# Kernel optimization log

Measured on AMD Instinct MI355X. Metric: run time of the kernel, lower is better.

## Reference

```python
import jax, jax.numpy as jnp
import numpy as np

N = 100000      # num mesh nodes
E = 600000      # num directed edges (avg degree ~6)
IN = 6          # input features
HID = 128       # hidden channels
HEADS = 8
CH = HID // HEADS  # 16 per-head channels
L = 4           # num GNN layers
OUT = 4


def layer_norm(x, w, b, eps=1e-5):
    m = x.mean(-1, keepdims=True)
    v = ((x - m) ** 2).mean(-1, keepdims=True)
    return (x - m) / jnp.sqrt(v + eps) * w + b


def setup_inputs() -> dict:
    key = jax.random.key(0)
    ks = jax.random.split(key, 24)
    s = 0.05
    inp = {
        "x": jax.random.normal(ks[0], (N, IN), jnp.float32),
        "edge_index": jax.random.randint(ks[1], (2, E), 0, N, jnp.int64),
        # input MLP: Linear(IN,HID) + LayerNorm
        "w_in": jax.random.normal(ks[2], (IN, HID), jnp.float32) * s,
        "b_in": jnp.zeros((HID,), jnp.float32),
        "ln_in_w": jnp.ones((HID,), jnp.float32),
        "ln_in_b": jnp.zeros((HID,), jnp.float32),
        # 4 GAT layers (stacked): W, att_src, att_dst, bias + per-layer LayerNorm
        "Wg": jax.random.normal(ks[3], (L, HID, HID), jnp.float32) * s,
        "a_src": jax.random.normal(ks[4], (L, HEADS, CH), jnp.float32) * s,
        "a_dst": jax.random.normal(ks[5], (L, HEADS, CH), jnp.float32) * s,
        "bg": jnp.zeros((L, HID), jnp.float32),
        "lnw": jnp.ones((L, HID), jnp.float32),
        "lnb": jnp.zeros((L, HID), jnp.float32),
        # output MLP: Linear(HID,HID)+LN+ReLU -> Linear(HID,HID//2)+ReLU -> Linear(HID//2,OUT)
        "w1": jax.random.normal(ks[6], (HID, HID), jnp.float32) * s,
        "b1": jnp.zeros((HID,), jnp.float32),
        "lnow": jnp.ones((HID,), jnp.float32),
        "lnob": jnp.zeros((HID,), jnp.float32),
        "w2": jax.random.normal(ks[7], (HID, HID // 2), jnp.float32) * s,
        "b2": jnp.zeros((HID // 2,), jnp.float32),
        "w3": jax.random.normal(ks[8], (HID // 2, OUT), jnp.float32) * s,
        "b3": jnp.zeros((OUT,), jnp.float32),
    }
    return inp


def reference(x, edge_index, w_in, b_in, ln_in_w, ln_in_b,
              Wg, a_src, a_dst, bg, lnw, lnb,
              w1, b1, lnow, lnob, w2, b2, w3, b3):
    # PyG GATConv adds self-loops by default
    loop = jnp.arange(N, dtype=edge_index.dtype)
    src = jnp.concatenate([edge_index[0], loop])  # message source
    dst = jnp.concatenate([edge_index[1], loop])  # message destination (softmax groups)

    h = jax.nn.relu(layer_norm(x @ w_in + b_in, ln_in_w, ln_in_b))  # (N, HID); dropout off (eval)

    for i in range(L):
        xw = (h @ Wg[i]).reshape(N, HEADS, CH)            # per-head transform
        al_s = (xw * a_src[i]).sum(-1)                    # (N, HEADS)
        al_d = (xw * a_dst[i]).sum(-1)                    # (N, HEADS)
        e = jax.nn.leaky_relu(al_s[src] + al_d[dst], 0.2) # (E+N, HEADS)
        # numerically stable segment softmax over incoming edges of each dst
        mx = jax.ops.segment_max(e, dst, num_segments=N)
        p = jnp.exp(e - mx[dst])
        denom = jax.ops.segment_sum(p, dst, num_segments=N)
        alpha = p / denom[dst]                            # attention dropout off (eval)
        msg = xw[src] * alpha[:, :, None]                 # (E+N, HEADS, CH)
        agg = jax.ops.segment_sum(msg, dst, num_segments=N).reshape(N, HID) + bg[i]
        h = h + jax.nn.relu(layer_norm(agg, lnw[i], lnb[i]))

    o = jax.nn.relu(layer_norm(h @ w1 + b1, lnow, lnob))
    o = jax.nn.relu(o @ w2 + b2)
    return o @ w3 + b3
```

## Files before the change

### kernel.cpp

```cpp
#include <hip/hip_runtime.h>
#include <hip/hip_bf16.h>

#define NN 100000
#define NE 600000

typedef __bf16 bf16x8 __attribute__((ext_vector_type(8)));
typedef __bf16 bf16x4 __attribute__((ext_vector_type(4)));
typedef float  f32x4  __attribute__((ext_vector_type(4)));

__device__ __forceinline__ float dot4(float4 a, float4 b){
  return a.x*b.x + a.y*b.y + a.z*b.z + a.w*b.w;
}
__device__ __forceinline__ void bf2f(unsigned v, float& a, float& b){
  union { unsigned u; float f; } ua, ub;
  ua.u = v << 16;
  ub.u = v & 0xFFFF0000u;
  a = ua.f; b = ub.f;
}
__device__ __forceinline__ void bf8f(uint4 v, float* r){
  bf2f(v.x, r[0], r[1]);
  bf2f(v.y, r[2], r[3]);
  bf2f(v.z, r[4], r[5]);
  bf2f(v.w, r[6], r[7]);
}

__global__ void count_edges(const int* __restrict__ dst, int* __restrict__ cnt){
  int e = blockIdx.x*256 + threadIdx.x;
  if (e < NE){
    unsigned d = (unsigned)dst[e];
    if (d < NN) atomicAdd(&cnt[d], 1);
  }
}

__global__ void scan1(const int* __restrict__ cnt, int* __restrict__ offs, int* __restrict__ bsum){
  __shared__ int sh[256];
  const int tid = threadIdx.x;
  const int base = blockIdx.x*2048 + tid*8;
  int pre[8]; int s = 0;
  #pragma unroll
  for (int j=0;j<8;j++){
    int idx = base + j;
    int v = (idx < NN) ? cnt[idx] : 0;
    pre[j] = s; s += v;
  }
  sh[tid] = s;
  __syncthreads();
  for (int d=1; d<256; d<<=1){
    int t = (tid >= d) ? sh[tid-d] : 0;
    __syncthreads();
    sh[tid] += t;
    __syncthreads();
  }
  int off = (tid > 0) ? sh[tid-1] : 0;
  #pragma unroll
  for (int j=0;j<8;j++){
    int idx = base + j;
    if (idx < NN) offs[idx] = off + pre[j];
  }
  if (tid == 255) bsum[blockIdx.x] = sh[255];
}

__global__ void scan2(int* __restrict__ bsum){
  if (threadIdx.x == 0){
    int s = 0;
    for (int i=0;i<49;i++){ int t = bsum[i]; bsum[i] = s; s += t; }
  }
}

__global__ void scan3(int* __restrict__ offs, const int* __restrict__ bsum, int* __restrict__ cursor){
  int i = blockIdx.x*256 + threadIdx.x;
  if (i < NN){
    int v = offs[i] + bsum[i>>11];
    offs[i] = v; cursor[i] = v;
  }
  if (i == 0) offs[NN] = NE;
}

__global__ void fill_csr(const int* __restrict__ src, const int* __restrict__ dst,
                         int* __restrict__ cursor, int* __restrict__ csrsrc){
  int e = blockIdx.x*256 + threadIdx.x;
  if (e < NE){
    unsigned d = (unsigned)dst[e];
    unsigned s = (unsigned)src[e];
    if (d < NN && s < NN){
      int p = atomicAdd(&cursor[d], 1);
      csrsrc[p] = (int)s;
    }
  }
}

__global__ void repack_w(const float* __restrict__ Wg, const float* __restrict__ w1,
                         const float* __restrict__ w2,
                         __bf16* __restrict__ phi, __bf16* __restrict__ plo)
{
  int gid = blockIdx.x*256 + threadIdx.x;
  const float* W; int C; size_t obase; int rem;
  if (gid < 8192)      { W = Wg + (size_t)(gid/2048)*16384; C = 128; obase = (size_t)(gid/2048)*16384; rem = gid % 2048; }
  else if (gid < 10240){ W = w1; C = 128; obase = 65536; rem = gid - 8192; }
  else if (gid < 11264){ W = w2; C = 64;  obase = 81920; rem = gid - 10240; }
  else return;
  const int lane = rem & 63;
  const int tks  = rem >> 6;
  const int ks = tks & 3, t = tks >> 2;
  const int col = t*16 + (lane & 15);
  const int kb  = ks*32 + (lane >> 4)*8;
  const size_t o = obase + (size_t)rem*8;
  #pragma unroll
  for (int j=0;j<8;j++){
    float v = W[(size_t)(kb+j)*C + col];
    __bf16 hb = (__bf16)v;
    phi[o+j] = hb;
    plo[o+j] = (__bf16)(v - (float)hb);
  }
}

__global__ __launch_bounds__(256) void input_mlp(const float* __restrict__ x,
    const float* __restrict__ win, const float* __restrict__ b,
    const float* __restrict__ lnw, const float* __restrict__ lnb,
    __bf16* __restrict__ h)
{
  const int tid = threadIdx.x;
  const int g = tid >> 5, l = tid & 31;
  const int n = blockIdx.x*8 + g;
  const float4* W4 = (const float4*)win;
  float xr[6];
  #pragma unroll
  for (int k=0;k<6;k++) xr[k] = x[n*6+k];
  float4 s = ((const float4*)b)[l];
  #pragma unroll
  for (int k=0;k<6;k++){
    float4 w = W4[k*32 + l];
    s.x = fmaf(xr[k], w.x, s.x);
    s.y = fmaf(xr[k], w.y, s.y);
    s.z = fmaf(xr[k], w.z, s.z);
    s.w = fmaf(xr[k], w.w, s.w);
  }
  float sum = s.x+s.y+s.z+s.w;
  float sq  = dot4(s,s);
  #pragma unroll
  for (int o=16;o>=1;o>>=1){ sum += __shfl_xor(sum,o); sq += __shfl_xor(sq,o); }
  float mean = sum*(1.f/128.f);
  float var  = sq*(1.f/128.f) - mean*mean;
  float rr = rsqrtf(var + 1e-5f);
  float4 lw = ((const float4*)lnw)[l];
  float4 lb = ((const float4*)lnb)[l];
  bf16x4 y;
  y[0] = (__bf16)fmaxf((s.x-mean)*rr*lw.x + lb.x, 0.f);
  y[1] = (__bf16)fmaxf((s.y-mean)*rr*lw.y + lb.y, 0.f);
  y[2] = (__bf16)fmaxf((s.z-mean)*rr*lw.z + lb.z, 0.f);
  y[3] = (__bf16)fmaxf((s.w-mean)*rr*lw.w + lb.w, 0.f);
  *(bf16x4*)(h + (size_t)n*128 + 4*l) = y;
}

template<int C, bool HAS_BIAS, bool DO_LN, bool DO_RELU, bool GAT, bool OUTP, bool SPLIT, bool SKIPLO, bool ABF16>
__global__ __launch_bounds__(256) void gemm_mfma(
    const float* __restrict__ Xf, const __bf16* __restrict__ Xb,
    const __bf16* __restrict__ Bhi, const __bf16* __restrict__ Blo,
    const float* __restrict__ bias,
    const float* __restrict__ lnw, const float* __restrict__ lnb,
    const float* __restrict__ asrc, const float* __restrict__ adst,
    float* __restrict__ Y, __bf16* __restrict__ Yb,
    float* __restrict__ als, float* __restrict__ ald,
    const float* __restrict__ w3, const float* __restrict__ b3,
    float* __restrict__ outp)
{
  constexpr int NT = SPLIT ? C/32 : C/16;
  const int tid = threadIdx.x;
  const int wid = tid >> 6, lane = tid & 63;
  const int lrow = lane & 15, lgrp = lane >> 4;
  const int m0    = SPLIT ? (blockIdx.x*32 + (wid>>1)*16) : ((blockIdx.x*4 + wid)*16);
  const int colt0 = SPLIT ? (wid & 1)*NT : 0;

  bf16x8 Ahi[4], Alo[4];
  {
    int row = m0 + lrow; if (row >= NN) row = NN-1;
    if constexpr (ABF16){
      const __bf16* Xr = Xb + (size_t)row*128 + lgrp*8;
      #pragma unroll
      for (int ks=0; ks<4; ks++) Ahi[ks] = *(const bf16x8*)(Xr + ks*32);
    } else {
      const float* Xr = Xf + (size_t)row*128 + lgrp*8;
      #pragma unroll
      for (int ks=0; ks<4; ks++){
        float4 u0 = *(const float4*)(Xr + ks*32);
        float4 u1 = *(const float4*)(Xr + ks*32 + 4);
        float v[8] = {u0.x,u0.y,u0.z,u0.w,u1.x,u1.y,u1.z,u1.w};
        bf16x8 h8, l8;
        #pragma unroll
        for (int j=0;j<8;j++){
          __bf16 hb = (__bf16)v[j];
          h8[j] = hb;
          l8[j] = (__bf16)(v[j] - (float)hb);
        }
        Ahi[ks] = h8; Alo[ks] = l8;
      }
    }
  }

  f32x4 acc[NT];
  #pragma unroll
  for (int t=0;t<NT;t++){ acc[t] = (f32x4){0.f,0.f,0.f,0.f}; }

  const bf16x8* B8h = (const bf16x8*)Bhi;
  const bf16x8* B8l = (const bf16x8*)Blo;
  #pragma unroll
  for (int ks=0;ks<4;ks++){
    bf16x8 bh[NT];
    #pragma unroll
    for (int t=0;t<NT;t++) bh[t] = B8h[((colt0+t)*4+ks)*64 + lane];
    #pragma unroll
    for (int t=0;t<NT;t++)
      acc[t] = __builtin_amdgcn_mfma_f32_16x16x32_bf16(Ahi[ks], bh[t], acc[t], 0,0,0);
    if constexpr (!ABF16){
      #pragma unroll
      for (int t=0;t<NT;t++)
        acc[t] = __builtin_amdgcn_mfma_f32_16x16x32_bf16(Alo[ks], bh[t], acc[t], 0,0,0);
    }
    if constexpr (!SKIPLO){
      #pragma unroll
      for (int t=0;t<NT;t++){
        bf16x8 bl = B8l[((colt0+t)*4+ks)*64 + lane];
        acc[t] = __builtin_amdgcn_mfma_f32_16x16x32_bf16(Ahi[ks], bl, acc[t], 0,0,0);
      }
    }
  }

  if constexpr (HAS_BIAS){
    #pragma unroll
    for (int t=0;t<NT;t++){
      float bv = bias[(colt0+t)*16 + lrow];
      #pragma unroll
      for (int i=0;i<4;i++) acc[t][i] += bv;
    }
  }

  if constexpr (GAT){
    #pragma unroll
    for (int t=0;t<NT;t++){
      float av = asrc[(colt0+t)*16 + lrow];
      float dv2 = adst[(colt0+t)*16 + lrow];
      float ps[4], pd[4];
      #pragma unroll
      for (int i=0;i<4;i++){
        int n = m0 + lgrp*4 + i;
        if (n < NN) Yb[(size_t)n*C + (colt0+t)*16 + lrow] = (__bf16)acc[t][i];
        ps[i] = acc[t][i]*av; pd[i] = acc[t][i]*dv2;
      }
      #pragma unroll
      for (int off=1; off<16; off<<=1){
        #pragma unroll
        for (int i=0;i<4;i++){
          ps[i] += __shfl_xor(ps[i], off);
          pd[i] += __shfl_xor(pd[i], off);
        }
      }
      if (lrow == 0){
        #pragma unroll
        for (int i=0;i<4;i++){
          int n = m0 + lgrp*4 + i;
          if (n < NN){ als[n*8 + colt0 + t] = ps[i]; ald[n*8 + colt0 + t] = pd[i]; }
        }
      }
    }
  } else {
    if constexpr (DO_LN){
      float s[4] = {0,0,0,0}, q[4] = {0,0,0,0};
      #pragma unroll
      for (int t=0;t<NT;t++){
        #pragma unroll
        for (int i=0;i<4;i++){ s[i] += acc[t][i]; q[i] += acc[t][i]*acc[t][i]; }
      }
      #pragma unroll
      for (int off=1; off<16; off<<=1){
        #pragma unroll
        for (int i=0;i<4;i++){ s[i] += __shfl_xor(s[i], off); q[i] += __shfl_xor(q[i], off); }
      }
      float mean[4], rr[4];
      #pragma unroll
      for (int i=0;i<4;i++){
        mean[i] = s[i]*(1.0f/C);
        float var = q[i]*(1.0f/C) - mean[i]*mean[i];
        rr[i] = rsqrtf(var + 1e-5f);
      }
      #pragma unroll
      for (int t=0;t<NT;t++){
        float lw = lnw[t*16 + lrow], lb = lnb[t*16 + lrow];
        #pragma unroll
        for (int i=0;i<4;i++){
          float v = (acc[t][i]-mean[i])*rr[i]*lw + lb;
          if constexpr (DO_RELU) v = fmaxf(v, 0.f);
          acc[t][i] = v;
        }
      }
    } else if constexpr (DO_RELU){
      #pragma unroll
      for (int t=0;t<NT;t++){
        #pragma unroll
        for (int i=0;i<4;i++) acc[t][i] = fmaxf(acc[t][i], 0.f);
      }
    }
    if constexpr (OUTP){
      float4 w3r[NT];
      #pragma unroll
      for (int t=0;t<NT;t++) w3r[t] = ((const float4*)w3)[t*16 + lrow];
      float4 b3v = *(const float4*)b3;
      #pragma unroll
      for (int i=0;i<4;i++){
        float4 po = make_float4(0.f,0.f,0.f,0.f);
        #pragma unroll
        for (int t=0;t<NT;t++){
          po.x = fmaf(acc[t][i], w3r[t].x, po.x);
          po.y = fmaf(acc[t][i], w3r[t].y, po.y);
          po.z = fmaf(acc[t][i], w3r[t].z, po.z);
          po.w = fmaf(acc[t][i], w3r[t].w, po.w);
        }
        #pragma unroll
        for (int off=1; off<16; off<<=1){
          po.x += __shfl_xor(po.x, off);
          po.y += __shfl_xor(po.y, off);
          po.z += __shfl_xor(po.z, off);
          po.w += __shfl_xor(po.w, off);
        }
        if (lrow == 0){
          int n = m0 + lgrp*4 + i;
          if (n < NN){
            float4 o;
            o.x = po.x + b3v.x; o.y = po.y + b3v.y;
            o.z = po.z + b3v.z; o.w = po.w + b3v.w;
            ((float4*)outp)[n] = o;
          }
        }
      }
    } else {
      #pragma unroll
      for (int t=0;t<NT;t++){
        #pragma unroll
        for (int i=0;i<4;i++){
          int n = m0 + lgrp*4 + i;
          if (n < NN) Y[(size_t)n*C + t*16 + lrow] = acc[t][i];
        }
      }
    }
  }
}

__global__ __launch_bounds__(256) void gat_aggregate(
    const __bf16* __restrict__ xw, const float* __restrict__ als, const float* __restrict__ ald,
    const int* __restrict__ offs, const int* __restrict__ csrsrc,
    const float* __restrict__ bg, const float* __restrict__ lnw, const float* __restrict__ lnb,
    __bf16* __restrict__ h)
{
  const int tid = threadIdx.x;
  const int grp = tid >> 4, sl = tid & 15;
  const int n = blockIdx.x*16 + grp;
  const int hh = sl >> 1;
  const float ad = ald[n*8 + hh];
  const uint4* xw128 = (const uint4*)xw;

  float t = als[n*8 + hh] + ad; t = t > 0.f ? t : 0.2f*t;
  float pp = __expf(t);
  float s = pp;
  float m[8];
  bf8f(xw128[(unsigned)n*16u + sl], m);
  float acc[8];
  #pragma unroll
  for (int c=0;c<8;c++) acc[c] = pp*m[c];

  const int start = offs[n], end = offs[n+1];
  int e = start;
  for (; e+4 <= end; e += 4){
    int s4[4]; float a[4]; uint4 x4[4];
    #pragma unroll
    for (int j=0;j<4;j++) s4[j] = csrsrc[e+j];
    #pragma unroll
    for (int j=0;j<4;j++){
      a[j]  = als[s4[j]*8 + hh];
      x4[j] = xw128[(unsigned)s4[j]*16u + sl];
    }
    #pragma unroll
    for (int j=0;j<4;j++){
      float u = a[j] + ad; u = u > 0.f ? u : 0.2f*u;
      float q = __expf(u);
      s += q;
      float mm[8];
      bf8f(x4[j], mm);
      #pragma unroll
      for (int c=0;c<8;c++) acc[c] = fmaf(q, mm[c], acc[c]);
    }
  }
  if (e+2 <= end){
    int sA = csrsrc[e], sB = csrsrc[e+1];
    float aA = als[sA*8+hh], aB = als[sB*8+hh];
    uint4 xA = xw128[(unsigned)sA*16u + sl];
    uint4 xB = xw128[(unsigned)sB*16u + sl];
    float u;
    u = aA+ad; u = u>0.f?u:0.2f*u; float qA = __expf(u);
    u = aB+ad; u = u>0.f?u:0.2f*u; float qB = __expf(u);
    s += qA+qB;
    float mA[8], mB[8];
    bf8f(xA, mA); bf8f(xB, mB);
    #pragma unroll
    for (int c=0;c<8;c++) acc[c] = fmaf(qA, mA[c], fmaf(qB, mB[c], acc[c]));
    e += 2;
  }
  if (e < end){
    int sA = csrsrc[e];
    float aA = als[sA*8+hh];
    uint4 xA = xw128[(unsigned)sA*16u + sl];
    float u = aA+ad; u = u>0.f?u:0.2f*u; float qA = __expf(u);
    s += qA;
    float mA[8];
    bf8f(xA, mA);
    #pragma unroll
    for (int c=0;c<8;c++) acc[c] = fmaf(qA, mA[c], acc[c]);
  }

  float4 bg0 = ((const float4*)bg)[2*sl];
  float4 bg1 = ((const float4*)bg)[2*sl+1];
  float bgv[8] = {bg0.x,bg0.y,bg0.z,bg0.w,bg1.x,bg1.y,bg1.z,bg1.w};
  float inv = 1.0f/s;
  float val[8];
  #pragma unroll
  for (int c=0;c<8;c++) val[c] = acc[c]*inv + bgv[c];
  float sum = 0.f, sq = 0.f;
  #pragma unroll
  for (int c=0;c<8;c++){ sum += val[c]; sq += val[c]*val[c]; }
  #pragma unroll
  for (int off=8; off>=1; off>>=1){ sum += __shfl_xor(sum,off); sq += __shfl_xor(sq,off); }
  float mean = sum*(1.f/128.f);
  float var  = sq*(1.f/128.f) - mean*mean;
  float rr = rsqrtf(var + 1e-5f);
  float4 lw0 = ((const float4*)lnw)[2*sl];
  float4 lw1 = ((const float4*)lnw)[2*sl+1];
  float4 lb0 = ((const float4*)lnb)[2*sl];
  float4 lb1 = ((const float4*)lnb)[2*sl+1];
  float lwv[8] = {lw0.x,lw0.y,lw0.z,lw0.w,lw1.x,lw1.y,lw1.z,lw1.w};
  float lbv[8] = {lb0.x,lb0.y,lb0.z,lb0.w,lb1.x,lb1.y,lb1.z,lb1.w};
  bf16x8* hp = (bf16x8*)(h + (size_t)n*128 + 8*sl);
  bf16x8 hv8 = *hp;
  bf16x8 ho;
  #pragma unroll
  for (int c=0;c<8;c++){
    float hv = (float)hv8[c] + fmaxf((val[c]-mean)*rr*lwv[c] + lbv[c], 0.f);
    ho[c] = (__bf16)hv;
  }
  *hp = ho;
}

extern "C" void kernel_launch(void* const* d_in, const int* in_sizes, int n_in,
                              void* d_out, int out_size, void* d_ws, size_t ws_size,
                              hipStream_t stream)
{
  const float* x       = (const float*)d_in[0];
  const int*   ei      = (const int*)d_in[1];
  const float* w_in    = (const float*)d_in[2];
  const float* b_in    = (const float*)d_in[3];
  const float* ln_in_w = (const float*)d_in[4];
  const float* ln_in_b = (const float*)d_in[5];
  const float* Wg      = (const float*)d_in[6];
  const float* a_src   = (const float*)d_in[7];
  const float* a_dst   = (const float*)d_in[8];
  const float* bg      = (const float*)d_in[9];
  const float* lnw     = (const float*)d_in[10];
  const float* lnb     = (const float*)d_in[11];
  const float* w1      = (const float*)d_in[12];
  const float* b1      = (const float*)d_in[13];
  const float* lnow    = (const float*)d_in[14];
  const float* lnob    = (const float*)d_in[15];
  const float* w2      = (const float*)d_in[16];
  const float* b2      = (const float*)d_in[17];
  const float* w3      = (const float*)d_in[18];
  const float* b3      = (const float*)d_in[19];
  float* out = (float*)d_out;

  char* p = (char*)d_ws;
  auto carve = [&](size_t bytes)->void*{
    void* r = (void*)p; p += (bytes + 255) & ~(size_t)255; return r;
  };
  __bf16* h   = (__bf16*)carve((size_t)NN*128*2);
  float* xw   = (float*)carve((size_t)NN*128*4);
  __bf16* xwb = (__bf16*)carve((size_t)NN*128*2);
  float* als  = (float*)carve((size_t)NN*8*4);
  float* ald  = (float*)carve((size_t)NN*8*4);
  int* offs   = (int*)carve((size_t)(NN+1)*4);
  int* cursor = (int*)carve((size_t)NN*4);
  int* cnt    = (int*)carve((size_t)NN*4);
  int* csrsrc = (int*)carve((size_t)NE*4);
  int* bsum   = (int*)carve(64*4);
  __bf16* pWhi = (__bf16*)carve((size_t)90112*2);
  __bf16* pWlo = (__bf16*)carve((size_t)90112*2);

  const int* esrc = ei;
  const int* edst = ei + NE;

  repack_w<<<44, 256, 0, stream>>>(Wg, w1, w2, pWhi, pWlo);

  hipMemsetAsync(cnt, 0, (size_t)NN*4, stream);
  count_edges<<<(NE+255)/256, 256, 0, stream>>>(edst, cnt);
  scan1<<<49, 256, 0, stream>>>(cnt, offs, bsum);
  scan2<<<1, 64, 0, stream>>>(bsum);
  scan3<<<(NN+255)/256, 256, 0, stream>>>(offs, bsum, cursor);
  fill_csr<<<(NE+255)/256, 256, 0, stream>>>(esrc, edst, cursor, csrsrc);

  input_mlp<<<NN/8, 256, 0, stream>>>(x, w_in, b_in, ln_in_w, ln_in_b, h);

  const int GRID  = (NN + 63) / 64;
  const int GRIDS = (NN + 31) / 32;
  for (int i=0;i<4;i++){
    gemm_mfma<128,false,false,false,true,false,true,true,true><<<GRIDS, 256, 0, stream>>>(
        nullptr, h, pWhi + (size_t)i*16384, pWlo + (size_t)i*16384, nullptr, nullptr, nullptr,
        a_src + i*128, a_dst + i*128, nullptr, xwb, als, ald, nullptr, nullptr, nullptr);
    gat_aggregate<<<NN/16, 256, 0, stream>>>(xwb, als, ald, offs, csrsrc,
        bg + i*128, lnw + i*128, lnb + i*128, h);
  }

  gemm_mfma<128,true,true,true,false,false,false,false,true><<<GRID, 256, 0, stream>>>(
      nullptr, h, pWhi + 65536, pWlo + 65536, b1, lnow, lnob, nullptr, nullptr, xw, nullptr,
      nullptr, nullptr, nullptr, nullptr, nullptr);
  gemm_mfma<64,true,false,true,false,true,false,false,false><<<GRID, 256, 0, stream>>>(
      xw, nullptr, pWhi + 81920, pWlo + 81920, b2, nullptr, nullptr, nullptr, nullptr, nullptr, nullptr,
      nullptr, nullptr, w3, b3, out);
}
```

Baseline: 411.4 us.

## Fold attention vectors into GAT weight and use 32x32 MFMA GEMM

Precomputes W·a_src and W·a_dst as 16 extra output columns of the per-layer weight, so the attention logits come straight out of the GEMM instead of being reduced with shuffles. The GAT projection moves to a new kernel built on 32x32x16 bf16 MFMA, with 128 rows per block and a fifth column tile holding the logits. The goal is to cut the epilogue shuffle work and raise MFMA efficiency. In exchange it does extra padded MFMA work on the logit tile, and the folded attention weights are rounded to bf16, which changes precision.

```diff
diff --git a/kernel.cpp b/kernel.cpp
--- a/kernel.cpp
+++ b/kernel.cpp
@@ -7,6 +7,7 @@
 typedef __bf16 bf16x8 __attribute__((ext_vector_type(8)));
 typedef __bf16 bf16x4 __attribute__((ext_vector_type(4)));
 typedef float  f32x4  __attribute__((ext_vector_type(4)));
+typedef float  f32x16 __attribute__((ext_vector_type(16)));
 
 __device__ __forceinline__ float dot4(float4 a, float4 b){
   return a.x*b.x + a.y*b.y + a.z*b.z + a.w*b.w;
@@ -114,6 +115,40 @@
   }
 }
 
+__global__ void repack_w32(const float* __restrict__ Wg,
+                           const float* __restrict__ a_src, const float* __restrict__ a_dst,
+                           __bf16* __restrict__ pb)
+{
+  int gid = blockIdx.x*256 + threadIdx.x;
+  if (gid >= 10240) return;
+  const int layer = gid / 2560, rem = gid % 2560;
+  const float* W = Wg + (size_t)layer*16384;
+  const int lane = rem & 63;
+  const int tks  = rem >> 6;
+  const int ks = tks & 7, t = tks >> 3;
+  const int kb  = ks*16 + (lane >> 5)*8;
+  const size_t o = (size_t)layer*20480 + (size_t)rem*8;
+  if (t < 4){
+    const int col = t*32 + (lane & 31);
+    #pragma unroll
+    for (int j=0;j<8;j++) pb[o+j] = (__bf16)W[(size_t)(kb+j)*128 + col];
+  } else {
+    const int cc = lane & 31;
+    #pragma unroll
+    for (int j=0;j<8;j++){
+      float v = 0.f;
+      if (cc < 16){
+        const int hd = cc & 7;
+        const float* av = (cc < 8 ? a_src : a_dst) + layer*128 + hd*16;
+        const int k = kb + j;
+        #pragma unroll
+        for (int c=0;c<16;c++) v += W[(size_t)k*128 + hd*16 + c] * av[c];
+      }
+      pb[o+j] = (__bf16)v;
+    }
+  }
+}
+
 __global__ __launch_bounds__(256) void input_mlp(const float* __restrict__ x,
     const float* __restrict__ win, const float* __restrict__ b,
     const float* __restrict__ lnw, const float* __restrict__ lnb,
@@ -152,24 +187,72 @@
   *(bf16x4*)(h + (size_t)n*128 + 4*l) = y;
 }
 
-template<int C, bool HAS_BIAS, bool DO_LN, bool DO_RELU, bool GAT, bool OUTP, bool SPLIT, bool SKIPLO, bool ABF16>
+__global__ __launch_bounds__(256) void gemm32_gat(const __bf16* __restrict__ X,
+    const __bf16* __restrict__ B32,
+    __bf16* __restrict__ Yb, float* __restrict__ als, float* __restrict__ ald)
+{
+  const int tid = threadIdx.x;
+  const int wid = tid >> 6, lane = tid & 63;
+  const int lm = lane & 31, lh = lane >> 5;
+  const int m0 = blockIdx.x*128 + wid*32;
+
+  f32x16 acc[5];
+  #pragma unroll
+  for (int t=0;t<5;t++){
+    #pragma unroll
+    for (int i=0;i<16;i++) acc[t][i] = 0.f;
+  }
+
+  int row = m0 + lm; if (row >= NN) row = NN-1;
+  const __bf16* Xr = X + (size_t)row*128 + lh*8;
+  const bf16x8* B8 = (const bf16x8*)B32;
+
+  #pragma unroll
+  for (int ks=0; ks<8; ks++){
+    bf16x8 a = *(const bf16x8*)(Xr + ks*16);
+    bf16x8 bh[5];
+    #pragma unroll
+    for (int t=0;t<5;t++) bh[t] = B8[(t*8+ks)*64 + lane];
+    #pragma unroll
+    for (int t=0;t<5;t++)
+      acc[t] = __builtin_amdgcn_mfma_f32_32x32x16_bf16(a, bh[t], acc[t], 0,0,0);
+  }
+
+  #pragma unroll
+  for (int t=0;t<4;t++){
+    #pragma unroll
+    for (int i=0;i<16;i++){
+      int r = (i&3) + 8*(i>>2) + 4*lh;
+      int n = m0 + r;
+      if (n < NN) Yb[(size_t)n*128 + t*32 + lm] = (__bf16)acc[t][i];
+    }
+  }
+  #pragma unroll
+  for (int i=0;i<16;i++){
+    int r = (i&3) + 8*(i>>2) + 4*lh;
+    int n = m0 + r;
+    if (n < NN){
+      if (lm < 8)       als[n*8 + lm]     = acc[4][i];
+      else if (lm < 16) ald[n*8 + lm - 8] = acc[4][i];
+    }
+  }
+}
+
+template<int C, bool DO_LN, bool DO_RELU, bool OUTP, bool ABF16>
 __global__ __launch_bounds__(256) void gemm_mfma(
     const float* __restrict__ Xf, const __bf16* __restrict__ Xb,
     const __bf16* __restrict__ Bhi, const __bf16* __restrict__ Blo,
     const float* __restrict__ bias,
     const float* __restrict__ lnw, const float* __restrict__ lnb,
-    const float* __restrict__ asrc, const float* __restrict__ adst,
-    float* __restrict__ Y, __bf16* __restrict__ Yb,
-    float* __restrict__ als, float* __restrict__ ald,
+    float* __restrict__ Y,
     const float* __restrict__ w3, const float* __restrict__ b3,
     float* __restrict__ outp)
 {
-  constexpr int NT = SPLIT ? C/32 : C/16;
+  constexpr int NT = C/16;
   const int tid = threadIdx.x;
   const int wid = tid >> 6, lane = tid & 63;
   const int lrow = lane & 15, lgrp = lane >> 4;
-  const int m0    = SPLIT ? (blockIdx.x*32 + (wid>>1)*16) : ((blockIdx.x*4 + wid)*16);
-  const int colt0 = SPLIT ? (wid & 1)*NT : 0;
+  const int m0 = (blockIdx.x*4 + wid)*16;
 
   bf16x8 Ahi[4], Alo[4];
   {
@@ -207,7 +290,7 @@
   for (int ks=0;ks<4;ks++){
     bf16x8 bh[NT];
     #pragma unroll
-    for (int t=0;t<NT;t++) bh[t] = B8h[((colt0+t)*4+ks)*64 + lane];
+    for (int t=0;t<NT;t++) bh[t] = B8h[(t*4+ks)*64 + lane];
     #pragma unroll
     for (int t=0;t<NT;t++)
       acc[t] = __builtin_amdgcn_mfma_f32_16x16x32_bf16(Ahi[ks], bh[t], acc[t], 0,0,0);
@@ -216,129 +299,97 @@
       for (int t=0;t<NT;t++)
         acc[t] = __builtin_amdgcn_mfma_f32_16x16x32_bf16(Alo[ks], bh[t], acc[t], 0,0,0);
     }
-    if constexpr (!SKIPLO){
+    {
       #pragma unroll
       for (int t=0;t<NT;t++){
-        bf16x8 bl = B8l[((colt0+t)*4+ks)*64 + lane];
+        bf16x8 bl = B8l[(t*4+ks)*64 + lane];
         acc[t] = __builtin_amdgcn_mfma_f32_16x16x32_bf16(Ahi[ks], bl, acc[t], 0,0,0);
       }
     }
   }
 
-  if constexpr (HAS_BIAS){
+  #pragma unroll
+  for (int t=0;t<NT;t++){
+    float bv = bias[t*16 + lrow];
+    #pragma unroll
+    for (int i=0;i<4;i++) acc[t][i] += bv;
+  }
+
+  if constexpr (DO_LN){
+    float s[4] = {0,0,0,0}, q[4] = {0,0,0,0};
     #pragma unroll
     for (int t=0;t<NT;t++){
-      float bv = bias[(colt0+t)*16 + lrow];
-      #pragma unroll
-      for (int i=0;i<4;i++) acc[t][i] += bv;
-    }
-  }
-
-  if constexpr (GAT){
+      #pragma unroll
+      for (int i=0;i<4;i++){ s[i] += acc[t][i]; q[i] += acc[t][i]*acc[t][i]; }
+    }
+    #pragma unroll
+    for (int off=1; off<16; off<<=1){
+      #pragma unroll
+      for (int i=0;i<4;i++){ s[i] += __shfl_xor(s[i], off); q[i] += __shfl_xor(q[i], off); }
+    }
+    float mean[4], rr[4];
+    #pragma unroll
+    for (int i=0;i<4;i++){
+      mean[i] = s[i]*(1.0f/C);
+      float var = q[i]*(1.0f/C) - mean[i]*mean[i];
+      rr[i] = rsqrtf(var + 1e-5f);
+    }
     #pragma unroll
     for (int t=0;t<NT;t++){
-      float av = asrc[(colt0+t)*16 + lrow];
-      float dv2 = adst[(colt0+t)*16 + lrow];
-      float ps[4], pd[4];
+      float lw = lnw[t*16 + lrow], lb = lnb[t*16 + lrow];
+      #pragma unroll
+      for (int i=0;i<4;i++){
+        float v = (acc[t][i]-mean[i])*rr[i]*lw + lb;
+        if constexpr (DO_RELU) v = fmaxf(v, 0.f);
+        acc[t][i] = v;
+      }
+    }
+  } else if constexpr (DO_RELU){
+    #pragma unroll
+    for (int t=0;t<NT;t++){
+      #pragma unroll
+      for (int i=0;i<4;i++) acc[t][i] = fmaxf(acc[t][i], 0.f);
+    }
+  }
+  if constexpr (OUTP){
+    float4 w3r[NT];
+    #pragma unroll
+    for (int t=0;t<NT;t++) w3r[t] = ((const float4*)w3)[t*16 + lrow];
+    float4 b3v = *(const float4*)b3;
+    #pragma unroll
+    for (int i=0;i<4;i++){
+      float4 po = make_float4(0.f,0.f,0.f,0.f);
+      #pragma unroll
+      for (int t=0;t<NT;t++){
+        po.x = fmaf(acc[t][i], w3r[t].x, po.x);
+        po.y = fmaf(acc[t][i], w3r[t].y, po.y);
+        po.z = fmaf(acc[t][i], w3r[t].z, po.z);
+        po.w = fmaf(acc[t][i], w3r[t].w, po.w);
+      }
+      #pragma unroll
+      for (int off=1; off<16; off<<=1){
+        po.x += __shfl_xor(po.x, off);
+        po.y += __shfl_xor(po.y, off);
+        po.z += __shfl_xor(po.z, off);
+        po.w += __shfl_xor(po.w, off);
+      }
+      if (lrow == 0){
+        int n = m0 + lgrp*4 + i;
+        if (n < NN){
+          float4 o;
+          o.x = po.x + b3v.x; o.y = po.y + b3v.y;
+          o.z = po.z + b3v.z; o.w = po.w + b3v.w;
+          ((float4*)outp)[n] = o;
+        }
+      }
+    }
+  } else {
+    #pragma unroll
+    for (int t=0;t<NT;t++){
       #pragma unroll
       for (int i=0;i<4;i++){
         int n = m0 + lgrp*4 + i;
-        if (n < NN) Yb[(size_t)n*C + (colt0+t)*16 + lrow] = (__bf16)acc[t][i];
-        ps[i] = acc[t][i]*av; pd[i] = acc[t][i]*dv2;
-      }
-      #pragma unroll
-      for (int off=1; off<16; off<<=1){
-        #pragma unroll
-        for (int i=0;i<4;i++){
-          ps[i] += __shfl_xor(ps[i], off);
-          pd[i] += __shfl_xor(pd[i], off);
-        }
-      }
-      if (lrow == 0){
-        #pragma unroll
-        for (int i=0;i<4;i++){
-          int n = m0 + lgrp*4 + i;
-          if (n < NN){ als[n*8 + colt0 + t] = ps[i]; ald[n*8 + colt0 + t] = pd[i]; }
-        }
-      }
-    }
-  } else {
-    if constexpr (DO_LN){
-      float s[4] = {0,0,0,0}, q[4] = {0,0,0,0};
-      #pragma unroll
-      for (int t=0;t<NT;t++){
-        #pragma unroll
-        for (int i=0;i<4;i++){ s[i] += acc[t][i]; q[i] += acc[t][i]*acc[t][i]; }
-      }
-      #pragma unroll
-      for (int off=1; off<16; off<<=1){
-        #pragma unroll
-        for (int i=0;i<4;i++){ s[i] += __shfl_xor(s[i], off); q[i] += __shfl_xor(q[i], off); }
-      }
-      float mean[4], rr[4];
-      #pragma unroll
-      for (int i=0;i<4;i++){
-        mean[i] = s[i]*(1.0f/C);
-        float var = q[i]*(1.0f/C) - mean[i]*mean[i];
-        rr[i] = rsqrtf(var + 1e-5f);
-      }
-      #pragma unroll
-      for (int t=0;t<NT;t++){
-        float lw = lnw[t*16 + lrow], lb = lnb[t*16 + lrow];
-        #pragma unroll
-        for (int i=0;i<4;i++){
-          float v = (acc[t][i]-mean[i])*rr[i]*lw + lb;
-          if constexpr (DO_RELU) v = fmaxf(v, 0.f);
-          acc[t][i] = v;
-        }
-      }
-    } else if constexpr (DO_RELU){
-      #pragma unroll
-      for (int t=0;t<NT;t++){
-        #pragma unroll
-        for (int i=0;i<4;i++) acc[t][i] = fmaxf(acc[t][i], 0.f);
-      }
-    }
-    if constexpr (OUTP){
-      float4 w3r[NT];
-      #pragma unroll
-      for (int t=0;t<NT;t++) w3r[t] = ((const float4*)w3)[t*16 + lrow];
-      float4 b3v = *(const float4*)b3;
-      #pragma unroll
-      for (int i=0;i<4;i++){
-        float4 po = make_float4(0.f,0.f,0.f,0.f);
-        #pragma unroll
-        for (int t=0;t<NT;t++){
-          po.x = fmaf(acc[t][i], w3r[t].x, po.x);
-          po.y = fmaf(acc[t][i], w3r[t].y, po.y);
-          po.z = fmaf(acc[t][i], w3r[t].z, po.z);
-          po.w = fmaf(acc[t][i], w3r[t].w, po.w);
-        }
-        #pragma unroll
-        for (int off=1; off<16; off<<=1){
-          po.x += __shfl_xor(po.x, off);
-          po.y += __shfl_xor(po.y, off);
-          po.z += __shfl_xor(po.z, off);
-          po.w += __shfl_xor(po.w, off);
-        }
-        if (lrow == 0){
-          int n = m0 + lgrp*4 + i;
-          if (n < NN){
-            float4 o;
-            o.x = po.x + b3v.x; o.y = po.y + b3v.y;
-            o.z = po.z + b3v.z; o.w = po.w + b3v.w;
-            ((float4*)outp)[n] = o;
-          }
-        }
-      }
-    } else {
-      #pragma unroll
-      for (int t=0;t<NT;t++){
-        #pragma unroll
-        for (int i=0;i<4;i++){
-          int n = m0 + lgrp*4 + i;
-          if (n < NN) Y[(size_t)n*C + t*16 + lrow] = acc[t][i];
-        }
+        if (n < NN) Y[(size_t)n*C + t*16 + lrow] = acc[t][i];
       }
     }
   }
@@ -489,11 +540,13 @@
   int* bsum   = (int*)carve(64*4);
   __bf16* pWhi = (__bf16*)carve((size_t)90112*2);
   __bf16* pWlo = (__bf16*)carve((size_t)90112*2);
+  __bf16* pW32 = (__bf16*)carve((size_t)4*20480*2);
 
   const int* esrc = ei;
   const int* edst = ei + NE;
 
   repack_w<<<44, 256, 0, stream>>>(Wg, w1, w2, pWhi, pWlo);
+  repack_w32<<<40, 256, 0, stream>>>(Wg, a_src, a_dst, pW32);
 
   hipMemsetAsync(cnt, 0, (size_t)NN*4, stream);
   count_edges<<<(NE+255)/256, 256, 0, stream>>>(edst, cnt);
@@ -504,20 +557,17 @@
 
   input_mlp<<<NN/8, 256, 0, stream>>>(x, w_in, b_in, ln_in_w, ln_in_b, h);
 
-  const int GRID  = (NN + 63) / 64;
-  const int GRIDS = (NN + 31) / 32;
+  const int GRID   = (NN + 63) / 64;
+  const int GRID32 = (NN + 127) / 128;
   for (int i=0;i<4;i++){
-    gemm_mfma<128,false,false,false,true,false,true,true,true><<<GRIDS, 256, 0, stream>>>(
-        nullptr, h, pWhi + (size_t)i*16384, pWlo + (size_t)i*16384, nullptr, nullptr, nullptr,
-        a_src + i*128, a_dst + i*128, nullptr, xwb, als, ald, nullptr, nullptr, nullptr);
+    gemm32_gat<<<GRID32, 256, 0, stream>>>(
+        h, pW32 + (size_t)i*20480, xwb, als, ald);
     gat_aggregate<<<NN/16, 256, 0, stream>>>(xwb, als, ald, offs, csrsrc,
         bg + i*128, lnw + i*128, lnb + i*128, h);
   }
 
-  gemm_mfma<128,true,true,true,false,false,false,false,true><<<GRID, 256, 0, stream>>>(
-      nullptr, h, pWhi + 65536, pWlo + 65536, b1, lnow, lnob, nullptr, nullptr, xw, nullptr,
-      nullptr, nullptr, nullptr, nullptr, nullptr);
-  gemm_mfma<64,true,false,true,false,true,false,false,false><<<GRID, 256, 0, stream>>>(
-      xw, nullptr, pWhi + 81920, pWlo + 81920, b2, nullptr, nullptr, nullptr, nullptr, nullptr, nullptr,
-      nullptr, nullptr, w3, b3, out);
-}
+  gemm_mfma<128,true,true,false,true><<<GRID, 256, 0, stream>>>(
+      nullptr, h, pWhi + 65536, pWlo + 65536, b1, lnow, lnob, xw, nullptr, nullptr, nullptr);
+  gemm_mfma<64,false,true,true,false><<<GRID, 256, 0, stream>>>(
+      xw, nullptr, pWhi + 81920, pWlo + 81920, b2, nullptr, nullptr, nullptr, w3, b3, out);
+}
```

New measurement: 407.1 us. Within noise of the previous version (-1.0%).
